# Optimization experiments

Measured on AMD Instinct MI355X. Metric: run time of the kernel, lower is better.

The kernel has to match this reference:

```python
import jax, jax.numpy as jnp
import numpy as np

B, F_, N, C, H = 32, 2048, 25, 3, 64  # batch, frames, nodes, in_channels, hidden_dim


def setup_inputs() -> dict:
    key = jax.random.key(0)
    k0, k1, k2, k3, k4 = jax.random.split(key, 5)
    x = jax.random.normal(k0, (B, C, F_, N), dtype=jnp.float32)
    mask = jax.random.randint(k1, (N, N), 0, 2).astype(jnp.float32)  # binary adjacency
    # nn.Linear(in_channels, hidden_dim)
    W = jax.random.normal(k2, (C, H), dtype=jnp.float32) / np.sqrt(C).astype(np.float32)
    bW = jnp.zeros((H,), dtype=jnp.float32)
    # nn.Linear(2*hidden_dim, 1) split into the half acting on h_i and the half on h_j
    a1 = jax.random.normal(k3, (H,), dtype=jnp.float32) / np.sqrt(2 * H).astype(np.float32)
    a2 = jax.random.normal(k4, (H,), dtype=jnp.float32) / np.sqrt(2 * H).astype(np.float32)
    ab = jnp.zeros((), dtype=jnp.float32)
    return {"x": x, "mask": mask, "W": W, "bW": bW, "a1": a1, "a2": a2, "ab": ab}


def reference(x, mask, W, bW, a1, a2, ab):
    # x: [B, C, F, N] -> [B, F, N, C]
    xp = jnp.transpose(x, (0, 2, 3, 1))
    h = xp @ W + bW                                  # [B, F, N, H]
    # score[b,f,i,j] = weight([h_i ; h_j]) = a1.h_i + a2.h_j + ab  (concat-linear decomposed)
    s1 = h @ a1                                      # [B, F, N]
    s2 = h @ a2                                      # [B, F, N]
    scores = s1[..., :, None] + s2[..., None, :] + ab  # [B, F, N, N]
    attn = jax.nn.softmax(scores, axis=-1)
    masked = attn * mask                             # broadcast [N,N]
    # torch.einsum('bfnn,bfnj->bfnj') takes the DIAGONAL of masked over its last two axes
    diag = jnp.diagonal(masked, axis1=-2, axis2=-1)  # [B, F, N]
    out = diag[..., None] * h                        # [B, F, N, H]
    return jnp.transpose(out, (0, 3, 1, 2))          # [B, H, F, N]
```

## Files before the change

### kernel.cpp

```cpp
#include <hip/hip_runtime.h>


typedef float vfloat4 __attribute__((ext_vector_type(4)));

namespace {
constexpr int B_ = 32, C_ = 3, F_ = 2048, N_ = 25, H_ = 64;
constexpr int FN   = F_ * N_;
constexpr int FN4  = FN / 4;
constexpr int THREADS = 256;
constexpr int JB   = FN4 / THREADS;
constexpr int MAXW = 264;
}

__global__ __launch_bounds__(THREADS) void gat_fused2(
    const float* __restrict__ x, const float* __restrict__ mask,
    const float* __restrict__ W, const float* __restrict__ bW,
    const float* __restrict__ a2, float* __restrict__ out)
{
  __shared__ float   xl[3][4 * MAXW];
  __shared__ float   dl[4 * MAXW];
  __shared__ vfloat4 Wp[H_];
  __shared__ float   mdl[N_];
  __shared__ float   wal[C_];

  const int tid = threadIdx.x;
  const int blk = blockIdx.x;
  const int b   = blk / JB;
  const int jb  = blk - b * JB;
  const int S   = jb * THREADS;
  const int p0  = S * 4;
  const int f0  = p0 / N_;
  const int f1  = (p0 + 4 * THREADS - 1) / N_;
  const int nf  = f1 - f0 + 1;
  const int A0  = (f0 * N_) & ~3;
  int A1 = (f1 * N_ + N_ + 3) & ~3;
  if (A1 > FN) A1 = FN;
  const int cnt4 = (A1 - A0) >> 2;

  const vfloat4* xg = (const vfloat4*)x;
#pragma unroll
  for (int c = 0; c < 3; ++c) {
    const vfloat4* src = xg + (size_t)(b * 3 + c) * FN4 + (A0 >> 2);
    vfloat4* dst = (vfloat4*)xl[c];
    for (int i = tid; i < cnt4; i += THREADS) dst[i] = src[i];
  }
  if (tid < H_) {
    vfloat4 w = {W[tid], W[H_ + tid], W[2 * H_ + tid], bW[tid]};
    Wp[tid] = w;
  } else if (tid < H_ + C_) {
    const int c = tid - H_;
    float s = 0.f;
    for (int h = 0; h < H_; ++h) s += W[c * H_ + h] * a2[h];
    wal[c] = s;
  }
  if (tid >= 128 && tid < 128 + N_) mdl[tid - 128] = mask[(tid - 128) * (N_ + 1)];
  __syncthreads();

  if (tid < nf) {
    const float wa0 = wal[0], wa1 = wal[1], wa2 = wal[2];
    const int base = (f0 + tid) * N_ - A0;
    float s[N_];
    float m = -3.0e38f;
#pragma unroll
    for (int n = 0; n < N_; ++n) {
      float v = fmaf(xl[2][base + n], wa2,
                fmaf(xl[1][base + n], wa1, xl[0][base + n] * wa0));
      s[n] = v;
      m = fmaxf(m, v);
    }
    float z = 0.f;
#pragma unroll
    for (int n = 0; n < N_; ++n) { s[n] = __expf(s[n] - m); z += s[n]; }
    const float inv = 1.f / z;
#pragma unroll
    for (int n = 0; n < N_; ++n) dl[base + n] = s[n] * inv * mdl[n];
  }
  __syncthreads();

  const int li = tid + S - (A0 >> 2);
  const vfloat4 x0 = ((const vfloat4*)xl[0])[li];
  const vfloat4 x1 = ((const vfloat4*)xl[1])[li];
  const vfloat4 x2 = ((const vfloat4*)xl[2])[li];
  const vfloat4 dd = ((const vfloat4*)dl)[li];

  vfloat4* og = (vfloat4*)out;
  const size_t ob = (size_t)b * H_ * FN4 + S + tid;
#pragma unroll 4
  for (int h = 0; h < H_; ++h) {
    const vfloat4 wv = Wp[h];
    vfloat4 o;
    o.x = dd.x * fmaf(x2.x, wv.z, fmaf(x1.x, wv.y, fmaf(x0.x, wv.x, wv.w)));
    o.y = dd.y * fmaf(x2.y, wv.z, fmaf(x1.y, wv.y, fmaf(x0.y, wv.x, wv.w)));
    o.z = dd.z * fmaf(x2.z, wv.z, fmaf(x1.z, wv.y, fmaf(x0.z, wv.x, wv.w)));
    o.w = dd.w * fmaf(x2.w, wv.z, fmaf(x1.w, wv.y, fmaf(x0.w, wv.x, wv.w)));
    __builtin_nontemporal_store(o, &og[ob + (size_t)h * FN4]);
  }
}

extern "C" void kernel_launch(void* const* d_in, const int* in_sizes, int n_in,
                              void* d_out, int out_size, void* d_ws, size_t ws_size,
                              hipStream_t stream) {
  const float* x    = (const float*)d_in[0];
  const float* mask = (const float*)d_in[1];
  const float* W    = (const float*)d_in[2];
  const float* bW   = (const float*)d_in[3];
  const float* a2   = (const float*)d_in[5];
  float* out = (float*)d_out;

  hipLaunchKernelGGL(gat_fused2, dim3(B_ * JB), dim3(THREADS), 0, stream,
                     x, mask, W, bW, a2, out);
}
```

Measured before the change: 81.97 us.

## Tile by whole frame blocks so each block owns 64 frames without halo

```diff
diff --git a/kernel.cpp b/kernel.cpp
--- a/kernel.cpp
+++ b/kernel.cpp
@@ -7,42 +7,37 @@
 constexpr int B_ = 32, C_ = 3, F_ = 2048, N_ = 25, H_ = 64;
 constexpr int FN   = F_ * N_;
 constexpr int FN4  = FN / 4;
+constexpr int TF   = 64;
+constexpr int TPOS = TF * N_;
+constexpr int TVEC = TPOS / 4;
 constexpr int THREADS = 256;
-constexpr int JB   = FN4 / THREADS;
-constexpr int MAXW = 264;
 }
 
-__global__ __launch_bounds__(THREADS) void gat_fused2(
+__global__ __launch_bounds__(THREADS) void gat_fused3(
     const float* __restrict__ x, const float* __restrict__ mask,
     const float* __restrict__ W, const float* __restrict__ bW,
     const float* __restrict__ a2, float* __restrict__ out)
 {
-  __shared__ float   xl[3][4 * MAXW];
-  __shared__ float   dl[4 * MAXW];
+  __shared__ vfloat4 x4[3][TVEC];
+  __shared__ vfloat4 d4[TVEC];
   __shared__ vfloat4 Wp[H_];
   __shared__ float   mdl[N_];
   __shared__ float   wal[C_];
 
   const int tid = threadIdx.x;
   const int blk = blockIdx.x;
-  const int b   = blk / JB;
-  const int jb  = blk - b * JB;
-  const int S   = jb * THREADS;
-  const int p0  = S * 4;
-  const int f0  = p0 / N_;
-  const int f1  = (p0 + 4 * THREADS - 1) / N_;
-  const int nf  = f1 - f0 + 1;
-  const int A0  = (f0 * N_) & ~3;
-  int A1 = (f1 * N_ + N_ + 3) & ~3;
-  if (A1 > FN) A1 = FN;
-  const int cnt4 = (A1 - A0) >> 2;
+  const int b   = blk >> 5;
+  const int ft  = blk & 31;
+  const size_t fbase4 = (size_t)ft * TVEC;
 
   const vfloat4* xg = (const vfloat4*)x;
-#pragma unroll
-  for (int c = 0; c < 3; ++c) {
-    const vfloat4* src = xg + (size_t)(b * 3 + c) * FN4 + (A0 >> 2);
-    vfloat4* dst = (vfloat4*)xl[c];
-    for (int i = tid; i < cnt4; i += THREADS) dst[i] = src[i];
+  {
+    vfloat4* dst = &x4[0][0];
+    for (int i = tid; i < 3 * TVEC; i += THREADS) {
+      const int c = i / TVEC;
+      const int j = i - c * TVEC;
+      dst[i] = xg[(size_t)(b * 3 + c) * FN4 + fbase4 + j];
+    }
   }
   if (tid < H_) {
     vfloat4 w = {W[tid], W[H_ + tid], W[2 * H_ + tid], bW[tid]};
@@ -56,15 +51,18 @@
   if (tid >= 128 && tid < 128 + N_) mdl[tid - 128] = mask[(tid - 128) * (N_ + 1)];
   __syncthreads();
 
-  if (tid < nf) {
+  if (tid < TF) {
+    const float* xl0 = (const float*)&x4[0][0];
+    const float* xl1 = (const float*)&x4[1][0];
+    const float* xl2 = (const float*)&x4[2][0];
     const float wa0 = wal[0], wa1 = wal[1], wa2 = wal[2];
-    const int base = (f0 + tid) * N_ - A0;
+    const int base = tid * N_;
     float s[N_];
     float m = -3.0e38f;
 #pragma unroll
     for (int n = 0; n < N_; ++n) {
-      float v = fmaf(xl[2][base + n], wa2,
-                fmaf(xl[1][base + n], wa1, xl[0][base + n] * wa0));
+      float v = fmaf(xl2[base + n], wa2,
+                fmaf(xl1[base + n], wa1, xl0[base + n] * wa0));
       s[n] = v;
       m = fmaxf(m, v);
     }
@@ -72,28 +70,44 @@
 #pragma unroll
     for (int n = 0; n < N_; ++n) { s[n] = __expf(s[n] - m); z += s[n]; }
     const float inv = 1.f / z;
+    float* dl = (float*)d4;
 #pragma unroll
     for (int n = 0; n < N_; ++n) dl[base + n] = s[n] * inv * mdl[n];
   }
   __syncthreads();
 
-  const int li = tid + S - (A0 >> 2);
-  const vfloat4 x0 = ((const vfloat4*)xl[0])[li];
-  const vfloat4 x1 = ((const vfloat4*)xl[1])[li];
-  const vfloat4 x2 = ((const vfloat4*)xl[2])[li];
-  const vfloat4 dd = ((const vfloat4*)dl)[li];
+  const bool has2 = tid < (TVEC - THREADS);
+  const vfloat4 xa0 = x4[0][tid];
+  const vfloat4 xa1 = x4[1][tid];
+  const vfloat4 xa2 = x4[2][tid];
+  const vfloat4 da  = d4[tid];
+  vfloat4 xb0 = {}, xb1 = {}, xb2 = {}, db = {};
+  if (has2) {
+    xb0 = x4[0][tid + THREADS];
+    xb1 = x4[1][tid + THREADS];
+    xb2 = x4[2][tid + THREADS];
+    db  = d4[tid + THREADS];
+  }
 
   vfloat4* og = (vfloat4*)out;
-  const size_t ob = (size_t)b * H_ * FN4 + S + tid;
+  const size_t ob = (size_t)b * H_ * FN4 + fbase4 + tid;
 #pragma unroll 4
   for (int h = 0; h < H_; ++h) {
     const vfloat4 wv = Wp[h];
     vfloat4 o;
-    o.x = dd.x * fmaf(x2.x, wv.z, fmaf(x1.x, wv.y, fmaf(x0.x, wv.x, wv.w)));
-    o.y = dd.y * fmaf(x2.y, wv.z, fmaf(x1.y, wv.y, fmaf(x0.y, wv.x, wv.w)));
-    o.z = dd.z * fmaf(x2.z, wv.z, fmaf(x1.z, wv.y, fmaf(x0.z, wv.x, wv.w)));
-    o.w = dd.w * fmaf(x2.w, wv.z, fmaf(x1.w, wv.y, fmaf(x0.w, wv.x, wv.w)));
+    o.x = da.x * fmaf(xa2.x, wv.z, fmaf(xa1.x, wv.y, fmaf(xa0.x, wv.x, wv.w)));
+    o.y = da.y * fmaf(xa2.y, wv.z, fmaf(xa1.y, wv.y, fmaf(xa0.y, wv.x, wv.w)));
+    o.z = da.z * fmaf(xa2.z, wv.z, fmaf(xa1.z, wv.y, fmaf(xa0.z, wv.x, wv.w)));
+    o.w = da.w * fmaf(xa2.w, wv.z, fmaf(xa1.w, wv.y, fmaf(xa0.w, wv.x, wv.w)));
     __builtin_nontemporal_store(o, &og[ob + (size_t)h * FN4]);
+    if (has2) {
+      vfloat4 o2;
+      o2.x = db.x * fmaf(xb2.x, wv.z, fmaf(xb1.x, wv.y, fmaf(xb0.x, wv.x, wv.w)));
+      o2.y = db.y * fmaf(xb2.y, wv.z, fmaf(xb1.y, wv.y, fmaf(xb0.y, wv.x, wv.w)));
+      o2.z = db.z * fmaf(xb2.z, wv.z, fmaf(xb1.z, wv.y, fmaf(xb0.z, wv.x, wv.w)));
+      o2.w = db.w * fmaf(xb2.w, wv.z, fmaf(xb1.w, wv.y, fmaf(xb0.w, wv.x, wv.w)));
+      __builtin_nontemporal_store(o2, &og[ob + (size_t)h * FN4 + THREADS]);
+    }
   }
 }
 
@@ -107,6 +121,6 @@
   const float* a2   = (const float*)d_in[5];
   float* out = (float*)d_out;
 
-  hipLaunchKernelGGL(gat_fused2, dim3(B_ * JB), dim3(THREADS), 0, stream,
+  hipLaunchKernelGGL(gat_fused3, dim3(B_ * (F_ / TF)), dim3(THREADS), 0, stream,
                      x, mask, W, bW, a2, out);
 }
```

After: 88.81 us. +8.3%, slower.

## Split into diag-precompute kernel and per-hidden-pair streaming write kernel

Applied to the files above, without the earlier changes.

```diff
diff --git a/kernel.cpp b/kernel.cpp
--- a/kernel.cpp
+++ b/kernel.cpp
@@ -7,7 +7,126 @@
 constexpr int B_ = 32, C_ = 3, F_ = 2048, N_ = 25, H_ = 64;
 constexpr int FN   = F_ * N_;
 constexpr int FN4  = FN / 4;
+constexpr int TF   = 64;
+constexpr int TPOS = TF * N_;
+constexpr int TVEC = TPOS / 4;
 constexpr int THREADS = 256;
+constexpr int STEPS = FN4 / THREADS;
+constexpr size_t D_BYTES = (size_t)B_ * FN * sizeof(float);
+}
+
+__global__ __launch_bounds__(THREADS) void gat_diag(
+    const float* __restrict__ x, const float* __restrict__ mask,
+    const float* __restrict__ W, const float* __restrict__ a2,
+    float* __restrict__ dout)
+{
+  __shared__ vfloat4 x4[3 * TVEC];
+  __shared__ vfloat4 d4[TVEC];
+  __shared__ float mdl[N_];
+  __shared__ float wal[C_];
+
+  const int tid = threadIdx.x;
+  const int blk = blockIdx.x;
+  const int b  = blk >> 5;
+  const int ft = blk & 31;
+  const size_t fbase = (size_t)ft * TPOS;
+
+  if (tid < N_) mdl[tid] = mask[tid * N_ + tid];
+  if (tid >= 64 && tid < 64 + C_) {
+    const int c = tid - 64;
+    float s = 0.f;
+    for (int h = 0; h < H_; ++h) s += W[c * H_ + h] * a2[h];
+    wal[c] = s;
+  }
+
+  const vfloat4* xg = (const vfloat4*)x;
+  for (int i = tid; i < 3 * TVEC; i += THREADS) {
+    int c = i / TVEC;
+    int j = i - c * TVEC;
+    x4[i] = xg[(size_t)(b * 3 + c) * FN4 + (fbase >> 2) + j];
+  }
+  __syncthreads();
+
+  if (tid < TF) {
+    const float* xl = (const float*)x4;
+    const float wa0 = wal[0], wa1 = wal[1], wa2 = wal[2];
+    const int base = tid * N_;
+    float s[N_];
+    float m = -3.0e38f;
+#pragma unroll
+    for (int n = 0; n < N_; ++n) {
+      float v = fmaf(xl[2 * TPOS + base + n], wa2,
+                fmaf(xl[TPOS + base + n], wa1, xl[base + n] * wa0));
+      s[n] = v;
+      m = fmaxf(m, v);
+    }
+    float z = 0.f;
+#pragma unroll
+    for (int n = 0; n < N_; ++n) { s[n] = __expf(s[n] - m); z += s[n]; }
+    const float inv = 1.f / z;
+    float* dl = (float*)d4;
+#pragma unroll
+    for (int n = 0; n < N_; ++n) dl[base + n] = s[n] * inv * mdl[n];
+  }
+  __syncthreads();
+
+  vfloat4* dg = (vfloat4*)dout;
+  const size_t db = ((size_t)b * FN + fbase) >> 2;
+  dg[db + tid] = d4[tid];
+  if (tid < TVEC - THREADS) dg[db + THREADS + tid] = d4[THREADS + tid];
+}
+
+__global__ __launch_bounds__(THREADS) void gat_write2(
+    const float* __restrict__ x, const float* __restrict__ d,
+    const float* __restrict__ W, const float* __restrict__ bW,
+    float* __restrict__ out)
+{
+  const int tid = threadIdx.x;
+  const int blk = blockIdx.x;
+  const int xcd = blk & 7;
+  const int idx = blk >> 3;
+  const int b   = xcd * 4 + (idx >> 5);
+  const int hp  = idx & 31;
+  const int h0  = hp * 2, h1 = h0 + 1;
+
+  const float w00 = W[h0], w01 = W[H_ + h0], w02 = W[2 * H_ + h0], bw0 = bW[h0];
+  const float w10 = W[h1], w11 = W[H_ + h1], w12 = W[2 * H_ + h1], bw1 = bW[h1];
+
+  const vfloat4* xg = (const vfloat4*)x;
+  const vfloat4* dg = (const vfloat4*)d;
+  vfloat4* og = (vfloat4*)out;
+
+  const size_t xb0 = (size_t)(b * 3 + 0) * FN4;
+  const size_t xb1 = (size_t)(b * 3 + 1) * FN4;
+  const size_t xb2 = (size_t)(b * 3 + 2) * FN4;
+  const size_t db  = (size_t)b * FN4;
+  const size_t ob0 = (size_t)(b * H_ + h0) * FN4;
+  const size_t ob1 = (size_t)(b * H_ + h1) * FN4;
+
+#pragma unroll 2
+  for (int s = 0; s < STEPS; ++s) {
+    const int j = s * THREADS + tid;
+    const vfloat4 x0 = xg[xb0 + j];
+    const vfloat4 x1 = xg[xb1 + j];
+    const vfloat4 x2 = xg[xb2 + j];
+    const vfloat4 dd = dg[db + j];
+    vfloat4 t;
+    t.x = fmaf(x2.x, w02, fmaf(x1.x, w01, fmaf(x0.x, w00, bw0)));
+    t.y = fmaf(x2.y, w02, fmaf(x1.y, w01, fmaf(x0.y, w00, bw0)));
+    t.z = fmaf(x2.z, w02, fmaf(x1.z, w01, fmaf(x0.z, w00, bw0)));
+    t.w = fmaf(x2.w, w02, fmaf(x1.w, w01, fmaf(x0.w, w00, bw0)));
+    vfloat4 o0 = {dd.x * t.x, dd.y * t.y, dd.z * t.z, dd.w * t.w};
+    __builtin_nontemporal_store(o0, &og[ob0 + j]);
+    t.x = fmaf(x2.x, w12, fmaf(x1.x, w11, fmaf(x0.x, w10, bw1)));
+    t.y = fmaf(x2.y, w12, fmaf(x1.y, w11, fmaf(x0.y, w10, bw1)));
+    t.z = fmaf(x2.z, w12, fmaf(x1.z, w11, fmaf(x0.z, w10, bw1)));
+    t.w = fmaf(x2.w, w12, fmaf(x1.w, w11, fmaf(x0.w, w10, bw1)));
+    vfloat4 o1 = {dd.x * t.x, dd.y * t.y, dd.z * t.z, dd.w * t.w};
+    __builtin_nontemporal_store(o1, &og[ob1 + j]);
+  }
+}
+
+namespace {
 constexpr int JB   = FN4 / THREADS;
 constexpr int MAXW = 264;
 }
@@ -107,6 +226,14 @@
   const float* a2   = (const float*)d_in[5];
   float* out = (float*)d_out;
 
-  hipLaunchKernelGGL(gat_fused2, dim3(B_ * JB), dim3(THREADS), 0, stream,
-                     x, mask, W, bW, a2, out);
-}
+  if (ws_size >= D_BYTES && d_ws != nullptr) {
+    float* d = (float*)d_ws;
+    hipLaunchKernelGGL(gat_diag, dim3(B_ * (F_ / TF)), dim3(THREADS), 0, stream,
+                       x, mask, W, a2, d);
+    hipLaunchKernelGGL(gat_write2, dim3(B_ * (H_ / 2)), dim3(THREADS), 0, stream,
+                       x, d, W, bW, out);
+  } else {
+    hipLaunchKernelGGL(gat_fused2, dim3(B_ * JB), dim3(THREADS), 0, stream,
+                       x, mask, W, bW, a2, out);
+  }
+}
```

Result: slower. 93.49 us (+14.1%).

## Process two tiles per block and prefetch second tile's input during first store loop

Applied to the files above, without the earlier changes.

```diff
diff --git a/kernel.cpp b/kernel.cpp
--- a/kernel.cpp
+++ b/kernel.cpp
@@ -9,10 +9,30 @@
 constexpr int FN4  = FN / 4;
 constexpr int THREADS = 256;
 constexpr int JB   = FN4 / THREADS;
+constexpr int NW   = B_ * JB;
+constexpr int BLOCKS = NW / 2;
 constexpr int MAXW = 264;
 }
 
-__global__ __launch_bounds__(THREADS) void gat_fused2(
+struct Geom { int b, S, nf, A0, cnt4; };
+
+__device__ __forceinline__ Geom mk_geom(int w) {
+  Geom g;
+  g.b = w / JB;
+  const int jb = w - g.b * JB;
+  g.S = jb * THREADS;
+  const int p0 = g.S * 4;
+  const int f0 = p0 / N_;
+  const int f1 = (p0 + 4 * THREADS - 1) / N_;
+  g.nf = f1 - f0 + 1;
+  g.A0 = (f0 * N_) & ~3;
+  int A1 = (f1 * N_ + N_ + 3) & ~3;
+  if (A1 > FN) A1 = FN;
+  g.cnt4 = (A1 - g.A0) >> 2;
+  return g;
+}
+
+__global__ __launch_bounds__(THREADS) void gat_pipe(
     const float* __restrict__ x, const float* __restrict__ mask,
     const float* __restrict__ W, const float* __restrict__ bW,
     const float* __restrict__ a2, float* __restrict__ out)
@@ -24,26 +44,9 @@
   __shared__ float   wal[C_];
 
   const int tid = threadIdx.x;
-  const int blk = blockIdx.x;
-  const int b   = blk / JB;
-  const int jb  = blk - b * JB;
-  const int S   = jb * THREADS;
-  const int p0  = S * 4;
-  const int f0  = p0 / N_;
-  const int f1  = (p0 + 4 * THREADS - 1) / N_;
-  const int nf  = f1 - f0 + 1;
-  const int A0  = (f0 * N_) & ~3;
-  int A1 = (f1 * N_ + N_ + 3) & ~3;
-  if (A1 > FN) A1 = FN;
-  const int cnt4 = (A1 - A0) >> 2;
+  const vfloat4* xg = (const vfloat4*)x;
+  vfloat4* og = (vfloat4*)out;
 
-  const vfloat4* xg = (const vfloat4*)x;
-#pragma unroll
-  for (int c = 0; c < 3; ++c) {
-    const vfloat4* src = xg + (size_t)(b * 3 + c) * FN4 + (A0 >> 2);
-    vfloat4* dst = (vfloat4*)xl[c];
-    for (int i = tid; i < cnt4; i += THREADS) dst[i] = src[i];
-  }
   if (tid < H_) {
     vfloat4 w = {W[tid], W[H_ + tid], W[2 * H_ + tid], bW[tid]};
     Wp[tid] = w;
@@ -54,11 +57,23 @@
     wal[c] = s;
   }
   if (tid >= 128 && tid < 128 + N_) mdl[tid - 128] = mask[(tid - 128) * (N_ + 1)];
+
+  const Geom g1 = mk_geom(blockIdx.x);
+#pragma unroll
+  for (int c = 0; c < 3; ++c) {
+    const vfloat4* src = xg + (size_t)(g1.b * 3 + c) * FN4 + (g1.A0 >> 2);
+    vfloat4* dst = (vfloat4*)xl[c];
+    for (int i = tid; i < g1.cnt4; i += THREADS) dst[i] = src[i];
+  }
   __syncthreads();
 
-  if (tid < nf) {
+  {
+    const int f0 = g1.A0 / N_ + ((g1.A0 % N_) ? 1 : 0);
+  }
+  if (tid < g1.nf) {
     const float wa0 = wal[0], wa1 = wal[1], wa2 = wal[2];
-    const int base = (f0 + tid) * N_ - A0;
+    const int f0 = (g1.S * 4) / N_;
+    const int base = (f0 + tid) * N_ - g1.A0;
     float s[N_];
     float m = -3.0e38f;
 #pragma unroll
@@ -77,23 +92,85 @@
   }
   __syncthreads();
 
-  const int li = tid + S - (A0 >> 2);
-  const vfloat4 x0 = ((const vfloat4*)xl[0])[li];
-  const vfloat4 x1 = ((const vfloat4*)xl[1])[li];
-  const vfloat4 x2 = ((const vfloat4*)xl[2])[li];
-  const vfloat4 dd = ((const vfloat4*)dl)[li];
+  const int li1 = tid + g1.S - (g1.A0 >> 2);
+  const vfloat4 x0 = ((const vfloat4*)xl[0])[li1];
+  const vfloat4 x1 = ((const vfloat4*)xl[1])[li1];
+  const vfloat4 x2 = ((const vfloat4*)xl[2])[li1];
+  const vfloat4 dd = ((const vfloat4*)dl)[li1];
 
-  vfloat4* og = (vfloat4*)out;
-  const size_t ob = (size_t)b * H_ * FN4 + S + tid;
+  const Geom g2 = mk_geom(blockIdx.x + BLOCKS);
+  const bool hv1 = (tid + THREADS) < g2.cnt4;
+  vfloat4 pf0a, pf1a, pf2a, pf0b = {}, pf1b = {}, pf2b = {};
+  {
+    const vfloat4* s0 = xg + (size_t)(g2.b * 3 + 0) * FN4 + (g2.A0 >> 2);
+    const vfloat4* s1 = xg + (size_t)(g2.b * 3 + 1) * FN4 + (g2.A0 >> 2);
+    const vfloat4* s2 = xg + (size_t)(g2.b * 3 + 2) * FN4 + (g2.A0 >> 2);
+    pf0a = s0[tid]; pf1a = s1[tid]; pf2a = s2[tid];
+    if (hv1) { pf0b = s0[tid + THREADS]; pf1b = s1[tid + THREADS]; pf2b = s2[tid + THREADS]; }
+  }
+
+  {
+    const size_t ob = (size_t)g1.b * H_ * FN4 + g1.S + tid;
 #pragma unroll 4
-  for (int h = 0; h < H_; ++h) {
-    const vfloat4 wv = Wp[h];
-    vfloat4 o;
-    o.x = dd.x * fmaf(x2.x, wv.z, fmaf(x1.x, wv.y, fmaf(x0.x, wv.x, wv.w)));
-    o.y = dd.y * fmaf(x2.y, wv.z, fmaf(x1.y, wv.y, fmaf(x0.y, wv.x, wv.w)));
-    o.z = dd.z * fmaf(x2.z, wv.z, fmaf(x1.z, wv.y, fmaf(x0.z, wv.x, wv.w)));
-    o.w = dd.w * fmaf(x2.w, wv.z, fmaf(x1.w, wv.y, fmaf(x0.w, wv.x, wv.w)));
-    __builtin_nontemporal_store(o, &og[ob + (size_t)h * FN4]);
+    for (int h = 0; h < H_; ++h) {
+      const vfloat4 wv = Wp[h];
+      vfloat4 o;
+      o.x = dd.x * fmaf(x2.x, wv.z, fmaf(x1.x, wv.y, fmaf(x0.x, wv.x, wv.w)));
+      o.y = dd.y * fmaf(x2.y, wv.z, fmaf(x1.y, wv.y, fmaf(x0.y, wv.x, wv.w)));
+      o.z = dd.z * fmaf(x2.z, wv.z, fmaf(x1.z, wv.y, fmaf(x0.z, wv.x, wv.w)));
+      o.w = dd.w * fmaf(x2.w, wv.z, fmaf(x1.w, wv.y, fmaf(x0.w, wv.x, wv.w)));
+      __builtin_nontemporal_store(o, &og[ob + (size_t)h * FN4]);
+    }
+  }
+
+  {
+    vfloat4* d0 = (vfloat4*)xl[0];
+    vfloat4* d1 = (vfloat4*)xl[1];
+    vfloat4* d2 = (vfloat4*)xl[2];
+    d0[tid] = pf0a; d1[tid] = pf1a; d2[tid] = pf2a;
+    if (hv1) { d0[tid + THREADS] = pf0b; d1[tid + THREADS] = pf1b; d2[tid + THREADS] = pf2b; }
+  }
+  __syncthreads();
+
+  if (tid < g2.nf) {
+    const float wa0 = wal[0], wa1 = wal[1], wa2 = wal[2];
+    const int f0 = (g2.S * 4) / N_;
+    const int base = (f0 + tid) * N_ - g2.A0;
+    float s[N_];
+    float m = -3.0e38f;
+#pragma unroll
+    for (int n = 0; n < N_; ++n) {
+      float v = fmaf(xl[2][base + n], wa2,
+                fmaf(xl[1][base + n], wa1, xl[0][base + n] * wa0));
+      s[n] = v;
+      m = fmaxf(m, v);
+    }
+    float z = 0.f;
+#pragma unroll
+    for (int n = 0; n < N_; ++n) { s[n] = __expf(s[n] - m); z += s[n]; }
+    const float inv = 1.f / z;
+#pragma unroll
+    for (int n = 0; n < N_; ++n) dl[base + n] = s[n] * inv * mdl[n];
+  }
+  __syncthreads();
+
+  {
+    const int li2 = tid + g2.S - (g2.A0 >> 2);
+    const vfloat4 y0 = ((const vfloat4*)xl[0])[li2];
+    const vfloat4 y1 = ((const vfloat4*)xl[1])[li2];
+    const vfloat4 y2 = ((const vfloat4*)xl[2])[li2];
+    const vfloat4 de = ((const vfloat4*)dl)[li2];
+    const size_t ob = (size_t)g2.b * H_ * FN4 + g2.S + tid;
+#pragma unroll 4
+    for (int h = 0; h < H_; ++h) {
+      const vfloat4 wv = Wp[h];
+      vfloat4 o;
+      o.x = de.x * fmaf(y2.x, wv.z, fmaf(y1.x, wv.y, fmaf(y0.x, wv.x, wv.w)));
+      o.y = de.y * fmaf(y2.y, wv.z, fmaf(y1.y, wv.y, fmaf(y0.y, wv.x, wv.w)));
+      o.z = de.z * fmaf(y2.z, wv.z, fmaf(y1.z, wv.y, fmaf(y0.z, wv.x, wv.w)));
+      o.w = de.w * fmaf(y2.w, wv.z, fmaf(y1.w, wv.y, fmaf(y0.w, wv.x, wv.w)));
+      __builtin_nontemporal_store(o, &og[ob + (size_t)h * FN4]);
+    }
   }
 }
 
@@ -107,6 +184,6 @@
   const float* a2   = (const float*)d_in[5];
   float* out = (float*)d_out;
 
-  hipLaunchKernelGGL(gat_fused2, dim3(B_ * JB), dim3(THREADS), 0, stream,
+  hipLaunchKernelGGL(gat_pipe, dim3(BLOCKS), dim3(THREADS), 0, stream,
                      x, mask, W, bW, a2, out);
 }
```

Result: slower. 85.42 us (+4.2%).
